# Kernel tuning notes

Hardware: AMD Instinct MI355X
Metric: run time of the kernel (lower is better)

The kernel has to match this reference:

```python
import jax, jax.numpy as jnp
import numpy as np

N = 2_000_000
F = 32  # feature_num
GH = GW = 256


def _bilinear_interpolate(grid, coords):
    # grid: [H, W, F], coords: [N, 2] in (0,1)
    W = grid.shape[1] - 1
    H = grid.shape[0] - 1
    x = coords[:, 0] * W
    y = coords[:, 1] * H
    x0 = x.astype(jnp.int32)
    y0 = y.astype(jnp.int32)
    xf = x % 1
    yf = y % 1
    x1 = jnp.minimum(x0 + 1, W)
    y1 = jnp.minimum(y0 + 1, H)
    tl = grid[y0, x0]  # [N, F]
    tr = grid[y0, x1]
    bl = grid[y1, x0]
    br = grid[y1, x1]
    top = (1 - xf)[:, None] * tl + xf[:, None] * tr
    bot = (1 - xf)[:, None] * bl + xf[:, None] * br
    return (1 - yf)[:, None] * top + yf[:, None] * bot


def setup_inputs() -> dict:
    key = jax.random.key(0)
    ks = jax.random.split(key, 16)
    inp = {
        "pos": jax.random.uniform(ks[0], (N, 2), dtype=jnp.float32),
        "dir": jax.random.uniform(ks[1], (N, 2), dtype=jnp.float32),
        # grids: randn * 10 as in the torch module
        "pos_grid": jax.random.normal(ks[2], (GH, GW, F), dtype=jnp.float32) * 10.0,
        "dir_grid": jax.random.normal(ks[3], (GH, GW, F), dtype=jnp.float32) * 10.0,
        # shared encoder: Linear(2,4), Linear(4,3)
        "enc_w1": jax.random.normal(ks[4], (2, 4), dtype=jnp.float32) * 0.5,
        "enc_b1": jax.random.normal(ks[5], (4,), dtype=jnp.float32) * 0.1,
        "enc_w2": jax.random.normal(ks[6], (4, 3), dtype=jnp.float32) * 0.5,
        "enc_b2": jax.random.normal(ks[7], (3,), dtype=jnp.float32) * 0.1,
        # fc head: 2F -> 64 -> 16 -> 8 -> 3
        "fc_w1": jax.random.normal(ks[8], (2 * F, 64), dtype=jnp.float32) * 0.1,
        "fc_b1": jnp.zeros((64,), dtype=jnp.float32),
        "fc_w2": jax.random.normal(ks[9], (64, 16), dtype=jnp.float32) * 0.1,
        "fc_b2": jnp.zeros((16,), dtype=jnp.float32),
        "fc_w3": jax.random.normal(ks[10], (16, 8), dtype=jnp.float32) * 0.1,
        "fc_b3": jnp.zeros((8,), dtype=jnp.float32),
        "fc_w4": jax.random.normal(ks[11], (8, 3), dtype=jnp.float32) * 0.1,
        "fc_b4": jnp.zeros((3,), dtype=jnp.float32),
    }
    return inp


def reference(pos, dir, pos_grid, dir_grid,
              enc_w1, enc_b1, enc_w2, enc_b2,
              fc_w1, fc_b1, fc_w2, fc_b2, fc_w3, fc_b3, fc_w4, fc_b4):
    def encoder(x):
        h = jnp.tanh(x @ enc_w1 + enc_b1)
        return jax.nn.sigmoid(h @ enc_w2 + enc_b2)  # [N, 3]; only cols 0,1 used

    p = encoder(pos)
    d = encoder(dir)
    # features are .detach()'ed in the original
    pos_feat = jax.lax.stop_gradient(_bilinear_interpolate(pos_grid, p))
    dir_feat = jax.lax.stop_gradient(_bilinear_interpolate(dir_grid, d))
    x = jnp.concatenate([pos_feat, dir_feat], axis=1)  # [N, 2F]
    # Dropout layers are identity in eval mode
    x = jax.nn.leaky_relu(x @ fc_w1 + fc_b1)
    x = jax.nn.leaky_relu(x @ fc_w2 + fc_b2)
    x = jax.nn.leaky_relu(x @ fc_w3 + fc_b3)
    x = jax.nn.leaky_relu(x @ fc_w4 + fc_b4)
    return jax.nn.sigmoid(x) * 255.0
```

## Files before the change

### kernel.cpp

```cpp
#include <hip/hip_runtime.h>
#include <math.h>

typedef __attribute__((ext_vector_type(8))) __bf16 bf16x8;
typedef __attribute__((ext_vector_type(4))) __bf16 bf16x4;
typedef __attribute__((ext_vector_type(4))) float floatx4;
typedef __attribute__((ext_vector_type(8))) float floatx8;

__device__ __forceinline__ float fast_rcp(float x) { return __builtin_amdgcn_rcpf(x); }
__device__ __forceinline__ float sigmoidf_(float z) { return fast_rcp(1.0f + __expf(-z)); }
__device__ __forceinline__ float fast_tanh(float z) {
    float e = __expf(2.0f * z);
    return 1.0f - 2.0f * fast_rcp(e + 1.0f);
}
__device__ __forceinline__ float leaky(float v) { return fmaxf(v, 0.01f * v); }

__device__ __forceinline__ int swzb(int row, int byteoff) {
    return row * 128 + (byteoff ^ ((row & 7) << 4));
}

__global__ void convert_grids(const float* __restrict__ g0, const float* __restrict__ g1,
                              const float* __restrict__ w1f, const float* __restrict__ w2f,
                              __bf16* __restrict__ o0, __bf16* __restrict__ o1,
                              __bf16* __restrict__ w1t, __bf16* __restrict__ w2t, int elems) {
    int i = blockIdx.x * blockDim.x + threadIdx.x;
    int nvec = elems >> 2;
    if (i < nvec) {
        float4 v = ((const float4*)g0)[i];
        bf16x4 r = { (__bf16)v.x, (__bf16)v.y, (__bf16)v.z, (__bf16)v.w };
        ((bf16x4*)o0)[i] = r;
    } else if (i < 2 * nvec) {
        int j = i - nvec;
        float4 v = ((const float4*)g1)[j];
        bf16x4 r = { (__bf16)v.x, (__bf16)v.y, (__bf16)v.z, (__bf16)v.w };
        ((bf16x4*)o1)[j] = r;
    } else {
        int j = i - 2 * nvec;
        if (j < 4096) {
            w1t[(j & 63) * 64 + (j >> 6)] = (__bf16)w1f[j];
        } else if (j < 4096 + 1024) {
            int k = j - 4096;
            w2t[(k & 15) * 64 + (k >> 4)] = (__bf16)w2f[k];
        }
    }
}

template<bool BF16G>
__global__ __launch_bounds__(256, BF16G ? 4 : 3) void gridnet_fwd(
    const float2* __restrict__ pos, const float2* __restrict__ dir_,
    const float* __restrict__ pos_gridf, const float* __restrict__ dir_gridf,
    const __bf16* __restrict__ pos_gridb, const __bf16* __restrict__ dir_gridb,
    const __bf16* __restrict__ W1t, const __bf16* __restrict__ W2t,
    const float* __restrict__ enc_w1, const float* __restrict__ enc_b1,
    const float* __restrict__ enc_w2, const float* __restrict__ enc_b2,
    const float* __restrict__ fc_w1, const float* __restrict__ fc_b1,
    const float* __restrict__ fc_w2, const float* __restrict__ fc_b2,
    const float* __restrict__ fc_w3, const float* __restrict__ fc_b3,
    const float* __restrict__ fc_w4, const float* __restrict__ fc_b4,
    float* __restrict__ out, int n)
{
    constexpr int XBYTES = 4 * 64 * 128;
    __shared__ __align__(16) char smem[BF16G ? XBYTES : XBYTES + 64 * 128 + 16 * 128];
    __shared__ float b1lds[64];
    __shared__ float b2lds[16];

    const int tid  = threadIdx.x;
    const int lane = tid & 63;
    const int wid  = tid >> 6;
    const int quad = lane >> 4;
    const int l15  = lane & 15;

    char* Xw = smem + wid * 64 * 128;
    char* W1p = smem + XBYTES;
    char* W2p = W1p + 64 * 128;

    if (!BF16G) {
        for (int idx = tid; idx < 4096; idx += 256)
            *(__bf16*)(W1p + swzb(idx & 63, (idx >> 6) * 2)) = (__bf16)fc_w1[idx];
        for (int idx = tid; idx < 1024; idx += 256)
            *(__bf16*)(W2p + swzb(idx & 15, (idx >> 4) * 2)) = (__bf16)fc_w2[idx];
    }
    if (tid < 64) b1lds[tid] = fc_b1[tid];
    if (tid < 16) b2lds[tid] = fc_b2[tid];
    __syncthreads();

    int i  = blockIdx.x * 256 + wid * 64 + lane;
    int ic = min(i, n - 1);

    int   ctl[2], ctr[2], cbl[2], cbr[2];
    float wtl[2], wtr[2], wbl[2], wbr[2];
    #pragma unroll
    for (int pass = 0; pass < 2; ++pass) {
        float2 xy = pass ? dir_[ic] : pos[ic];
        float hh[4];
        #pragma unroll
        for (int k = 0; k < 4; ++k)
            hh[k] = fast_tanh(xy.x * enc_w1[k] + xy.y * enc_w1[4 + k] + enc_b1[k]);
        float e0 = enc_b2[0], e1 = enc_b2[1];
        #pragma unroll
        for (int k = 0; k < 4; ++k) {
            e0 += hh[k] * enc_w2[3 * k + 0];
            e1 += hh[k] * enc_w2[3 * k + 1];
        }
        float x = sigmoidf_(e0) * 255.0f;
        float y = sigmoidf_(e1) * 255.0f;
        int x0 = (int)x, y0 = (int)y;
        float xf = x - (float)x0, yf = y - (float)y0;
        int x1 = min(x0 + 1, 255), y1 = min(y0 + 1, 255);
        float oxf = 1.0f - xf, oyf = 1.0f - yf;
        wtl[pass] = oyf * oxf; wtr[pass] = oyf * xf;
        wbl[pass] = yf * oxf;  wbr[pass] = yf * xf;
        ctl[pass] = ((y0 << 8) + x0) << 5; ctr[pass] = ((y0 << 8) + x1) << 5;
        cbl[pass] = ((y1 << 8) + x0) << 5; cbr[pass] = ((y1 << 8) + x1) << 5;
    }

    #pragma unroll
    for (int pass = 0; pass < 2; ++pass) {
        if (BF16G) {
            const __bf16* g = pass ? dir_gridb : pos_gridb;
            bf16x8 A[4], B[4], C[4], D[4];
            #pragma unroll
            for (int c = 0; c < 4; ++c) A[c] = *(const bf16x8*)(g + ctl[pass] + c * 8);
            #pragma unroll
            for (int c = 0; c < 4; ++c) B[c] = *(const bf16x8*)(g + ctr[pass] + c * 8);
            #pragma unroll
            for (int c = 0; c < 4; ++c) C[c] = *(const bf16x8*)(g + cbl[pass] + c * 8);
            #pragma unroll
            for (int c = 0; c < 4; ++c) D[c] = *(const bf16x8*)(g + cbr[pass] + c * 8);
            #pragma unroll
            for (int c = 0; c < 4; ++c) {
                floatx8 r = wtl[pass] * __builtin_convertvector(A[c], floatx8)
                          + wtr[pass] * __builtin_convertvector(B[c], floatx8)
                          + wbl[pass] * __builtin_convertvector(C[c], floatx8)
                          + wbr[pass] * __builtin_convertvector(D[c], floatx8);
                *(bf16x8*)(Xw + swzb(lane, pass * 64 + c * 16)) = __builtin_convertvector(r, bf16x8);
            }
        } else {
            const float* g = pass ? dir_gridf : pos_gridf;
            #pragma unroll
            for (int c = 0; c < 4; ++c) {
                floatx8 fa = *(const floatx8*)(g + ctl[pass] + c * 8);
                floatx8 fb = *(const floatx8*)(g + ctr[pass] + c * 8);
                floatx8 fc = *(const floatx8*)(g + cbl[pass] + c * 8);
                floatx8 fd = *(const floatx8*)(g + cbr[pass] + c * 8);
                floatx8 r = wtl[pass] * fa + wtr[pass] * fb + wbl[pass] * fc + wbr[pass] * fd;
                *(bf16x8*)(Xw + swzb(lane, pass * 64 + c * 16)) = __builtin_convertvector(r, bf16x8);
            }
        }
    }

    __asm__ volatile("s_waitcnt lgkmcnt(0)" ::: "memory");

    bf16x8 wf[2][4];
    #pragma unroll
    for (int ks = 0; ks < 2; ++ks)
        #pragma unroll
        for (int mt = 0; mt < 4; ++mt) {
            if (BF16G)
                wf[ks][mt] = *(const bf16x8*)(W1t + (mt * 16 + l15) * 64 + ks * 32 + quad * 8);
            else
                wf[ks][mt] = *(const bf16x8*)(W1p + swzb(mt * 16 + l15, ks * 64 + quad * 16));
        }

    floatx4 b1v[4];
    #pragma unroll
    for (int mt = 0; mt < 4; ++mt)
        b1v[mt] = *(const floatx4*)(b1lds + mt * 16 + quad * 4);

    floatx4 acc[4][4];
    #pragma unroll
    for (int mt = 0; mt < 4; ++mt)
        #pragma unroll
        for (int nt = 0; nt < 4; ++nt)
            acc[mt][nt] = b1v[mt];

    #pragma unroll
    for (int ks = 0; ks < 2; ++ks) {
        bf16x8 xf[4];
        #pragma unroll
        for (int nt = 0; nt < 4; ++nt)
            xf[nt] = *(const bf16x8*)(Xw + swzb(nt * 16 + l15, ks * 64 + quad * 16));
        #pragma unroll
        for (int mt = 0; mt < 4; ++mt)
            #pragma unroll
            for (int nt = 0; nt < 4; ++nt)
                acc[mt][nt] = __builtin_amdgcn_mfma_f32_16x16x32_bf16(wf[ks][mt], xf[nt], acc[mt][nt], 0, 0, 0);
    }

    #pragma unroll
    for (int mt = 0; mt < 4; ++mt)
        #pragma unroll
        for (int nt = 0; nt < 4; ++nt) {
            bf16x4 hv;
            #pragma unroll
            for (int r = 0; r < 4; ++r)
                hv[r] = (__bf16)leaky(acc[mt][nt][r]);
            *(bf16x4*)(Xw + swzb(nt * 16 + l15, mt * 32 + quad * 8)) = hv;
        }
    __asm__ volatile("s_waitcnt lgkmcnt(0)" ::: "memory");

    bf16x8 w2f[2];
    #pragma unroll
    for (int ks = 0; ks < 2; ++ks) {
        if (BF16G)
            w2f[ks] = *(const bf16x8*)(W2t + l15 * 64 + ks * 32 + quad * 8);
        else
            w2f[ks] = *(const bf16x8*)(W2p + swzb(l15, ks * 64 + quad * 16));
    }
    floatx4 b2v = *(const floatx4*)(b2lds + quad * 4);
    floatx4 acc2[4];
    #pragma unroll
    for (int nt = 0; nt < 4; ++nt) acc2[nt] = b2v;
    #pragma unroll
    for (int ks = 0; ks < 2; ++ks) {
        #pragma unroll
        for (int nt = 0; nt < 4; ++nt) {
            bf16x8 hf = *(const bf16x8*)(Xw + swzb(nt * 16 + l15, ks * 64 + quad * 16));
            acc2[nt] = __builtin_amdgcn_mfma_f32_16x16x32_bf16(w2f[ks], hf, acc2[nt], 0, 0, 0);
        }
    }

    #pragma unroll
    for (int nt = 0; nt < 4; ++nt) {
        floatx4 hv;
        #pragma unroll
        for (int r = 0; r < 4; ++r)
            hv[r] = leaky(acc2[nt][r]);
        *(floatx4*)(Xw + swzb(nt * 16 + l15, quad * 16)) = hv;
    }
    __asm__ volatile("s_waitcnt lgkmcnt(0)" ::: "memory");

    float h2[16];
    #pragma unroll
    for (int c = 0; c < 4; ++c) {
        floatx4 v = *(const floatx4*)(Xw + swzb(lane, c * 16));
        h2[4 * c + 0] = v[0]; h2[4 * c + 1] = v[1]; h2[4 * c + 2] = v[2]; h2[4 * c + 3] = v[3];
    }
    float h3[8];
    #pragma unroll
    for (int j = 0; j < 8; ++j) h3[j] = fc_b3[j];
    #pragma unroll
    for (int k = 0; k < 16; ++k) {
        float xv = h2[k];
        #pragma unroll
        for (int j = 0; j < 8; ++j) h3[j] = fmaf(xv, fc_w3[(k << 3) + j], h3[j]);
    }
    #pragma unroll
    for (int j = 0; j < 8; ++j) h3[j] = leaky(h3[j]);

    float o[3];
    #pragma unroll
    for (int j = 0; j < 3; ++j) o[j] = fc_b4[j];
    #pragma unroll
    for (int k = 0; k < 8; ++k) {
        float xv = h3[k];
        #pragma unroll
        for (int j = 0; j < 3; ++j) o[j] = fmaf(xv, fc_w4[3 * k + j], o[j]);
    }
    if (i < n) {
        #pragma unroll
        for (int j = 0; j < 3; ++j)
            out[3 * i + j] = sigmoidf_(leaky(o[j])) * 255.0f;
    }
}

extern "C" void kernel_launch(void* const* d_in, const int* in_sizes, int n_in,
                              void* d_out, int out_size, void* d_ws, size_t ws_size,
                              hipStream_t stream) {
    int n = in_sizes[0] / 2;
    const int GELEMS = 256 * 256 * 32;
    const int WELEMS = 4096 + 1024;
    bool use_bf16 = ws_size >= (size_t)((2 * GELEMS + WELEMS) * sizeof(__bf16));
    __bf16* g0  = (__bf16*)d_ws;
    __bf16* g1  = g0 + GELEMS;
    __bf16* w1t = g1 + GELEMS;
    __bf16* w2t = w1t + 4096;

    if (use_bf16) {
        int total = 2 * (GELEMS / 4) + WELEMS;
        convert_grids<<<(total + 255) / 256, 256, 0, stream>>>(
            (const float*)d_in[2], (const float*)d_in[3],
            (const float*)d_in[8], (const float*)d_in[10],
            g0, g1, w1t, w2t, GELEMS);
    }

    int blocks = (n + 255) / 256;
    if (use_bf16) {
        gridnet_fwd<true><<<blocks, 256, 0, stream>>>(
            (const float2*)d_in[0], (const float2*)d_in[1],
            (const float*)d_in[2], (const float*)d_in[3], g0, g1, w1t, w2t,
            (const float*)d_in[4], (const float*)d_in[5],
            (const float*)d_in[6], (const float*)d_in[7],
            (const float*)d_in[8], (const float*)d_in[9],
            (const float*)d_in[10], (const float*)d_in[11],
            (const float*)d_in[12], (const float*)d_in[13],
            (const float*)d_in[14], (const float*)d_in[15],
            (float*)d_out, n);
    } else {
        gridnet_fwd<false><<<blocks, 256, 0, stream>>>(
            (const float2*)d_in[0], (const float2*)d_in[1],
            (const float*)d_in[2], (const float*)d_in[3], g0, g1, w1t, w2t,
            (const float*)d_in[4], (const float*)d_in[5],
            (const float*)d_in[6], (const float*)d_in[7],
            (const float*)d_in[8], (const float*)d_in[9],
            (const float*)d_in[10], (const float*)d_in[11],
            (const float*)d_in[12], (const float*)d_in[13],
            (const float*)d_in[14], (const float*)d_in[15],
            (float*)d_out, n);
    }
}
```

Before: 249.5 us.

## Stage bilinear grid gathers through LDS with double-buffered async global-to-LDS loads

Replaces the per-lane register gathers of the four bf16 grid corners with cooperative global_load_lds transfers into a per-wave double-buffered LDS staging area. Each 16-point chunk is prefetched while the previous one is interpolated, with lanes reassigned by shuffling packed corner coordinates and fractional weights. The fc weights are now always converted into swizzled LDS inside the kernel, dropping the precomputed workspace copies. LDS grows to about 74 KB per block and launch bounds drop to 2 blocks per SM, which lowers occupancy and adds shuffle and LDS traffic.

```diff
diff --git a/kernel.cpp b/kernel.cpp
--- a/kernel.cpp
+++ b/kernel.cpp
@@ -18,10 +18,13 @@
     return row * 128 + (byteoff ^ ((row & 7) << 4));
 }
 
+__device__ __forceinline__ void gload_lds16(const __bf16* g, char* l) {
+    __builtin_amdgcn_global_load_lds((const __attribute__((address_space(1))) void*)g,
+                                     (__attribute__((address_space(3))) void*)l, 16, 0, 0);
+}
+
 __global__ void convert_grids(const float* __restrict__ g0, const float* __restrict__ g1,
-                              const float* __restrict__ w1f, const float* __restrict__ w2f,
-                              __bf16* __restrict__ o0, __bf16* __restrict__ o1,
-                              __bf16* __restrict__ w1t, __bf16* __restrict__ w2t, int elems) {
+                              __bf16* __restrict__ o0, __bf16* __restrict__ o1, int elems) {
     int i = blockIdx.x * blockDim.x + threadIdx.x;
     int nvec = elems >> 2;
     if (i < nvec) {
@@ -33,23 +36,14 @@
         float4 v = ((const float4*)g1)[j];
         bf16x4 r = { (__bf16)v.x, (__bf16)v.y, (__bf16)v.z, (__bf16)v.w };
         ((bf16x4*)o1)[j] = r;
-    } else {
-        int j = i - 2 * nvec;
-        if (j < 4096) {
-            w1t[(j & 63) * 64 + (j >> 6)] = (__bf16)w1f[j];
-        } else if (j < 4096 + 1024) {
-            int k = j - 4096;
-            w2t[(k & 15) * 64 + (k >> 4)] = (__bf16)w2f[k];
-        }
     }
 }
 
 template<bool BF16G>
-__global__ __launch_bounds__(256, BF16G ? 4 : 3) void gridnet_fwd(
+__global__ __launch_bounds__(256, 2) void gridnet_fwd(
     const float2* __restrict__ pos, const float2* __restrict__ dir_,
     const float* __restrict__ pos_gridf, const float* __restrict__ dir_gridf,
     const __bf16* __restrict__ pos_gridb, const __bf16* __restrict__ dir_gridb,
-    const __bf16* __restrict__ W1t, const __bf16* __restrict__ W2t,
     const float* __restrict__ enc_w1, const float* __restrict__ enc_b1,
     const float* __restrict__ enc_w2, const float* __restrict__ enc_b2,
     const float* __restrict__ fc_w1, const float* __restrict__ fc_b1,
@@ -58,8 +52,7 @@
     const float* __restrict__ fc_w4, const float* __restrict__ fc_b4,
     float* __restrict__ out, int n)
 {
-    constexpr int XBYTES = 4 * 64 * 128;
-    __shared__ __align__(16) char smem[BF16G ? XBYTES : XBYTES + 64 * 128 + 16 * 128];
+    __shared__ __align__(1024) char smem[32768 + 32768 + 8192 + 2048];
     __shared__ float b1lds[64];
     __shared__ float b2lds[16];
 
@@ -69,16 +62,15 @@
     const int quad = lane >> 4;
     const int l15  = lane & 15;
 
-    char* Xw = smem + wid * 64 * 128;
-    char* W1p = smem + XBYTES;
-    char* W2p = W1p + 64 * 128;
-
-    if (!BF16G) {
-        for (int idx = tid; idx < 4096; idx += 256)
-            *(__bf16*)(W1p + swzb(idx & 63, (idx >> 6) * 2)) = (__bf16)fc_w1[idx];
-        for (int idx = tid; idx < 1024; idx += 256)
-            *(__bf16*)(W2p + swzb(idx & 15, (idx >> 4) * 2)) = (__bf16)fc_w2[idx];
-    }
+    char* Xw  = smem + wid * 8192;
+    char* Stg = smem + 32768 + wid * 8192;
+    char* W1p = smem + 65536;
+    char* W2p = smem + 65536 + 8192;
+
+    for (int idx = tid; idx < 4096; idx += 256)
+        *(__bf16*)(W1p + swzb(idx & 63, (idx >> 6) * 2)) = (__bf16)fc_w1[idx];
+    for (int idx = tid; idx < 1024; idx += 256)
+        *(__bf16*)(W2p + swzb(idx & 15, (idx >> 4) * 2)) = (__bf16)fc_w2[idx];
     if (tid < 64) b1lds[tid] = fc_b1[tid];
     if (tid < 16) b2lds[tid] = fc_b2[tid];
     __syncthreads();
@@ -86,8 +78,8 @@
     int i  = blockIdx.x * 256 + wid * 64 + lane;
     int ic = min(i, n - 1);
 
-    int   ctl[2], ctr[2], cbl[2], cbr[2];
-    float wtl[2], wtr[2], wbl[2], wbr[2];
+    unsigned pcp[2];
+    float xfp[2], yfp[2];
     #pragma unroll
     for (int pass = 0; pass < 2; ++pass) {
         float2 xy = pass ? dir_[ic] : pos[ic];
@@ -104,47 +96,85 @@
         float x = sigmoidf_(e0) * 255.0f;
         float y = sigmoidf_(e1) * 255.0f;
         int x0 = (int)x, y0 = (int)y;
-        float xf = x - (float)x0, yf = y - (float)y0;
+        xfp[pass] = x - (float)x0;
+        yfp[pass] = y - (float)y0;
         int x1 = min(x0 + 1, 255), y1 = min(y0 + 1, 255);
-        float oxf = 1.0f - xf, oyf = 1.0f - yf;
-        wtl[pass] = oyf * oxf; wtr[pass] = oyf * xf;
-        wbl[pass] = yf * oxf;  wbr[pass] = yf * xf;
-        ctl[pass] = ((y0 << 8) + x0) << 5; ctr[pass] = ((y0 << 8) + x1) << 5;
-        cbl[pass] = ((y1 << 8) + x0) << 5; cbr[pass] = ((y1 << 8) + x1) << 5;
-    }
-
-    #pragma unroll
-    for (int pass = 0; pass < 2; ++pass) {
-        if (BF16G) {
-            const __bf16* g = pass ? dir_gridb : pos_gridb;
-            bf16x8 A[4], B[4], C[4], D[4];
+        pcp[pass] = (unsigned)x0 | ((unsigned)y0 << 8) | ((unsigned)x1 << 16) | ((unsigned)y1 << 24);
+    }
+
+    if (BF16G) {
+        const int m3 = lane & 3;
+        const int ck = (lane >> 2) & 3;
+        const int cc = lane >> 4;
+        const int bq = lane >> 2;
+        const int bk = lane & 3;
+
+        {
             #pragma unroll
-            for (int c = 0; c < 4; ++c) A[c] = *(const bf16x8*)(g + ctl[pass] + c * 8);
-            #pragma unroll
-            for (int c = 0; c < 4; ++c) B[c] = *(const bf16x8*)(g + ctr[pass] + c * 8);
-            #pragma unroll
-            for (int c = 0; c < 4; ++c) C[c] = *(const bf16x8*)(g + cbl[pass] + c * 8);
-            #pragma unroll
-            for (int c = 0; c < 4; ++c) D[c] = *(const bf16x8*)(g + cbr[pass] + c * 8);
+            for (int j = 0; j < 4; ++j) {
+                unsigned pcq = (unsigned)__shfl((int)pcp[0], j * 4 + m3);
+                int xq = (cc & 1) ? ((pcq >> 16) & 255) : (pcq & 255);
+                int yq = (cc & 2) ? (int)(pcq >> 24) : (int)((pcq >> 8) & 255);
+                gload_lds16(pos_gridb + ((yq << 8) + xq) * 32 + ck * 8, Stg + j * 1024);
+            }
+        }
+
+        #pragma unroll
+        for (int it = 0; it < 8; ++it) {
+            const int pass = it >> 2, j16 = it & 3;
+            const int buf = (it & 1) * 4096;
+            if (it < 7) {
+                const int nit = it + 1, np = nit >> 2, nj16 = nit & 3;
+                const __bf16* g = np ? dir_gridb : pos_gridb;
+                #pragma unroll
+                for (int j = 0; j < 4; ++j) {
+                    unsigned pcq = (unsigned)__shfl((int)pcp[np], nj16 * 16 + j * 4 + m3);
+                    int xq = (cc & 1) ? ((pcq >> 16) & 255) : (pcq & 255);
+                    int yq = (cc & 2) ? (int)(pcq >> 24) : (int)((pcq >> 8) & 255);
+                    gload_lds16(g + ((yq << 8) + xq) * 32 + ck * 8,
+                                Stg + ((nit & 1) * 4096) + j * 1024);
+                }
+            }
+            float xfq = __shfl(xfp[pass], j16 * 16 + bq);
+            float yfq = __shfl(yfp[pass], j16 * 16 + bq);
+            float oxf = 1.0f - xfq, oyf = 1.0f - yfq;
+            float w0 = oyf * oxf, w1 = oyf * xfq, w2 = yfq * oxf, w3 = yfq * xfq;
+
+            if (it < 7) __asm__ volatile("s_waitcnt vmcnt(4)" ::: "memory");
+            else        __asm__ volatile("s_waitcnt vmcnt(0)" ::: "memory");
+
+            const char* sb = Stg + buf + (lane >> 4) * 1024 + bk * 64 + ((lane >> 2) & 3) * 16;
+            bf16x8 c0 = *(const bf16x8*)(sb + 0);
+            bf16x8 c1 = *(const bf16x8*)(sb + 256);
+            bf16x8 c2 = *(const bf16x8*)(sb + 512);
+            bf16x8 c3 = *(const bf16x8*)(sb + 768);
+            floatx8 r = w0 * __builtin_convertvector(c0, floatx8)
+                      + w1 * __builtin_convertvector(c1, floatx8)
+                      + w2 * __builtin_convertvector(c2, floatx8)
+                      + w3 * __builtin_convertvector(c3, floatx8);
+            int q = j16 * 16 + bq;
+            *(bf16x8*)(Xw + swzb(q, pass * 64 + bk * 16)) = __builtin_convertvector(r, bf16x8);
+        }
+    } else {
+        #pragma unroll
+        for (int pass = 0; pass < 2; ++pass) {
+            const float* g = pass ? dir_gridf : pos_gridf;
+            unsigned pcq = pcp[pass];
+            int x0 = pcq & 255, y0 = (pcq >> 8) & 255, x1 = (pcq >> 16) & 255, y1 = pcq >> 24;
+            float xfq = xfp[pass], yfq = yfp[pass];
+            float oxf = 1.0f - xfq, oyf = 1.0f - yfq;
+            float w0 = oyf * oxf, w1 = oyf * xfq, w2 = yfq * oxf, w3 = yfq * xfq;
+            int ctl = ((y0 << 8) + x0) << 5, ctr = ((y0 << 8) + x1) << 5;
+            int cbl = ((y1 << 8) + x0) << 5, cbr = ((y1 << 8) + x1) << 5;
             #pragma unroll
             for (int c = 0; c < 4; ++c) {
-                floatx8 r = wtl[pass] * __builtin_convertvector(A[c], floatx8)
-                          + wtr[pass] * __builtin_convertvector(B[c], floatx8)
-                          + wbl[pass] * __builtin_convertvector(C[c], floatx8)
-                          + wbr[pass] * __builtin_convertvector(D[c], floatx8);
+                floatx8 fa = *(const floatx8*)(g + ctl + c * 8);
+                floatx8 fb = *(const floatx8*)(g + ctr + c * 8);
+                floatx8 fc = *(const floatx8*)(g + cbl + c * 8);
+                floatx8 fd = *(const floatx8*)(g + cbr + c * 8);
+                floatx8 r = w0 * fa + w1 * fb + w2 * fc + w3 * fd;
                 *(bf16x8*)(Xw + swzb(lane, pass * 64 + c * 16)) = __builtin_convertvector(r, bf16x8);
             }
-        } else {
-            const float* g = pass ? dir_gridf : pos_gridf;
-            #pragma unroll
-            for (int c = 0; c < 4; ++c) {
-                floatx8 fa = *(const floatx8*)(g + ctl[pass] + c * 8);
-                floatx8 fb = *(const floatx8*)(g + ctr[pass] + c * 8);
-                floatx8 fc = *(const floatx8*)(g + cbl[pass] + c * 8);
-                floatx8 fd = *(const floatx8*)(g + cbr[pass] + c * 8);
-                floatx8 r = wtl[pass] * fa + wtr[pass] * fb + wbl[pass] * fc + wbr[pass] * fd;
-                *(bf16x8*)(Xw + swzb(lane, pass * 64 + c * 16)) = __builtin_convertvector(r, bf16x8);
-            }
         }
     }
 
@@ -154,12 +184,8 @@
     #pragma unroll
     for (int ks = 0; ks < 2; ++ks)
         #pragma unroll
-        for (int mt = 0; mt < 4; ++mt) {
-            if (BF16G)
-                wf[ks][mt] = *(const bf16x8*)(W1t + (mt * 16 + l15) * 64 + ks * 32 + quad * 8);
-            else
-                wf[ks][mt] = *(const bf16x8*)(W1p + swzb(mt * 16 + l15, ks * 64 + quad * 16));
-        }
+        for (int mt = 0; mt < 4; ++mt)
+            wf[ks][mt] = *(const bf16x8*)(W1p + swzb(mt * 16 + l15, ks * 64 + quad * 16));
 
     floatx4 b1v[4];
     #pragma unroll
@@ -200,12 +226,8 @@
 
     bf16x8 w2f[2];
     #pragma unroll
-    for (int ks = 0; ks < 2; ++ks) {
-        if (BF16G)
-            w2f[ks] = *(const bf16x8*)(W2t + l15 * 64 + ks * 32 + quad * 8);
-        else
-            w2f[ks] = *(const bf16x8*)(W2p + swzb(l15, ks * 64 + quad * 16));
-    }
+    for (int ks = 0; ks < 2; ++ks)
+        w2f[ks] = *(const bf16x8*)(W2p + swzb(l15, ks * 64 + quad * 16));
     floatx4 b2v = *(const floatx4*)(b2lds + quad * 4);
     floatx4 acc2[4];
     #pragma unroll
@@ -268,26 +290,21 @@
                               hipStream_t stream) {
     int n = in_sizes[0] / 2;
     const int GELEMS = 256 * 256 * 32;
-    const int WELEMS = 4096 + 1024;
-    bool use_bf16 = ws_size >= (size_t)((2 * GELEMS + WELEMS) * sizeof(__bf16));
-    __bf16* g0  = (__bf16*)d_ws;
-    __bf16* g1  = g0 + GELEMS;
-    __bf16* w1t = g1 + GELEMS;
-    __bf16* w2t = w1t + 4096;
+    bool use_bf16 = ws_size >= (size_t)(2 * GELEMS * sizeof(__bf16));
+    __bf16* g0 = (__bf16*)d_ws;
+    __bf16* g1 = g0 + GELEMS;
 
     if (use_bf16) {
-        int total = 2 * (GELEMS / 4) + WELEMS;
+        int total = 2 * (GELEMS / 4);
         convert_grids<<<(total + 255) / 256, 256, 0, stream>>>(
-            (const float*)d_in[2], (const float*)d_in[3],
-            (const float*)d_in[8], (const float*)d_in[10],
-            g0, g1, w1t, w2t, GELEMS);
+            (const float*)d_in[2], (const float*)d_in[3], g0, g1, GELEMS);
     }
 
     int blocks = (n + 255) / 256;
     if (use_bf16) {
         gridnet_fwd<true><<<blocks, 256, 0, stream>>>(
             (const float2*)d_in[0], (const float2*)d_in[1],
-            (const float*)d_in[2], (const float*)d_in[3], g0, g1, w1t, w2t,
+            (const float*)d_in[2], (const float*)d_in[3], g0, g1,
             (const float*)d_in[4], (const float*)d_in[5],
             (const float*)d_in[6], (const float*)d_in[7],
             (const float*)d_in[8], (const float*)d_in[9],
@@ -298,7 +315,7 @@
     } else {
         gridnet_fwd<false><<<blocks, 256, 0, stream>>>(
             (const float2*)d_in[0], (const float2*)d_in[1],
-            (const float*)d_in[2], (const float*)d_in[3], g0, g1, w1t, w2t,
+            (const float*)d_in[2], (const float*)d_in[3], g0, g1,
             (const float*)d_in[4], (const float*)d_in[5],
             (const float*)d_in[6], (const float*)d_in[7],
             (const float*)d_in[8], (const float*)d_in[9],
```

Measured after the change: 255.6 us. 1.02x slower.
